# Kernel optimization log

Hardware: AMD Instinct MI355X
Metric: run time of the kernel (lower is better)

Reference implementation:

```python
import jax, jax.numpy as jnp
import numpy as np

NEG = -1e30  # log-space 'minus infinity' that stays finite in fp32 arithmetic
BLANK = 0


def _lse3(a, b, c):
    m = jnp.maximum(jnp.maximum(a, b), c)
    return m + jnp.log(jnp.exp(a - m) + jnp.exp(b - m) + jnp.exp(c - m))


def setup_inputs() -> dict:
    key = jax.random.key(0)
    k1, k2, k3, k4 = jax.random.split(key, 4)
    B, T, C, L = 16, 512, 4096, 128
    scores = jax.random.normal(k1, (B, T, C), dtype=jnp.float32)
    labels = jax.random.randint(k2, (B, L), 1, C, dtype=jnp.int64)      # no blanks in targets
    feat_lens = jax.random.randint(k3, (B,), 384, T + 1, dtype=jnp.int64)
    label_lens = jax.random.randint(k4, (B,), 64, L + 1, dtype=jnp.int64)
    return {"scores": scores, "labels": labels, "feat_lens": feat_lens, "label_lens": label_lens}


def reference(scores, labels, feat_lens, label_lens):
    # scores: [B, T, C]. Matches torch: log_softmax then nn.CTCLoss(blank=0,
    # reduction='mean', zero_infinity=True).
    scores = scores.astype(jnp.float32)
    log_probs = jax.nn.log_softmax(scores, axis=-1)                      # [B, T, C]
    B, T, C = scores.shape
    L = labels.shape[1]
    S = 2 * L + 1  # extended label: blank, l1, blank, ..., lL, blank

    ext = jnp.full((B, S), BLANK, dtype=labels.dtype).at[:, 1::2].set(labels)
    # Gather per-(t, extended-symbol) log-probs once: [B, T, S]
    lp = jnp.take_along_axis(log_probs, jnp.broadcast_to(ext[:, None, :], (B, T, S)), axis=2)

    # skip transition s-2 -> s allowed iff ext[s] != blank and ext[s] != ext[s-2]
    skip = jnp.concatenate(
        [jnp.zeros((B, 2), bool), (ext[:, 2:] != ext[:, :-2]) & (ext[:, 2:] != BLANK)], axis=1)

    alpha0 = jnp.full((B, S), NEG, dtype=jnp.float32).at[:, 0].set(lp[:, 0, 0])
    alpha0 = alpha0.at[:, 1].set(jnp.where(label_lens > 0, lp[:, 0, 1], NEG))

    lp_t_first = jnp.swapaxes(lp, 0, 1)  # [T, B, S]

    def step(alpha, xs):
        lp_t, t = xs
        a1 = jnp.pad(alpha, ((0, 0), (1, 0)), constant_values=NEG)[:, :S]
        a2 = jnp.pad(alpha, ((0, 0), (2, 0)), constant_values=NEG)[:, :S]
        a2 = jnp.where(skip, a2, NEG)
        new = lp_t + _lse3(alpha, a1, a2)
        alpha = jnp.where((t < feat_lens)[:, None], new, alpha)  # freeze past feat_len
        return alpha, None

    alpha, _ = jax.lax.scan(step, alpha0, (lp_t_first[1:], jnp.arange(1, T)))

    end = 2 * label_lens  # index of final blank per sample
    a_end = jnp.take_along_axis(alpha, end[:, None], axis=1)[:, 0]
    a_end1 = jnp.where(
        label_lens > 0,
        jnp.take_along_axis(alpha, jnp.maximum(end - 1, 0)[:, None], axis=1)[:, 0], NEG)
    m = jnp.maximum(a_end, a_end1)
    log_lik = m + jnp.log(jnp.exp(a_end - m) + jnp.exp(a_end1 - m))
    loss = -log_lik
    loss = jnp.where(loss > 0.5e30, 0.0, loss)  # zero_infinity=True
    denom = jnp.maximum(label_lens, 1).astype(loss.dtype)
    return jnp.mean(loss / denom)  # torch 'mean': divide by target_lengths, then batch mean
```

## Files before the change

kernel.cpp:

```cpp
#include <hip/hip_runtime.h>

#define T_ 512
#define C_ 4096
#define L_ 128
#define RCPLN2 1.4426950408889634f
#define LN2 0.6931471805599453f
#define NEGL (-1e30f)
#define SCALE_CTR 4.722366482869645e21f
#define SCALE_LOG 72.0f

__device__ __forceinline__ float fexp2(float x) { return __builtin_amdgcn_exp2f(x); }
__device__ __forceinline__ float flog2(float x) { return __builtin_amdgcn_logf(x); }
__device__ __forceinline__ float frcp(float x)  { return __builtin_amdgcn_rcpf(x); }
__device__ __forceinline__ float lg(float x)    { return (x > 0.f) ? flog2(x) : NEGL; }

template <int CTRL>
__device__ __forceinline__ float dppmov(float v) {
  return __int_as_float(__builtin_amdgcn_update_dpp(
      0, __float_as_int(v), CTRL, 0xF, 0xF, true));
}
__device__ __forceinline__ float wshr1(float v) { return dppmov<0x138>(v); }
__device__ __forceinline__ float wshl1(float v) { return dppmov<0x130>(v); }
template <int CTRL>
__device__ __forceinline__ float maxdpp(float v) {
  return fmaxf(v, dppmov<CTRL>(v));
}
__device__ __forceinline__ float wavemax(float v) {
  v = maxdpp<0xB1>(v);
  v = maxdpp<0x4E>(v);
  v = maxdpp<0x141>(v);
  v = maxdpp<0x140>(v);
  v = maxdpp<0x142>(v);
  v = maxdpp<0x143>(v);
  return __int_as_float(__builtin_amdgcn_readlane(__float_as_int(v), 63));
}

__global__ __launch_bounds__(256) void k_lse_gather(
    const float* __restrict__ scores, const int* __restrict__ labels,
    const int* __restrict__ feat_lens,
    float* __restrict__ p_lab, float* __restrict__ p_blank,
    int* __restrict__ dpDone, float* __restrict__ lossAcc) {
  const int row = blockIdx.x;
  const int b = row >> 9;
  const int t = row & (T_ - 1);
  if (row == 0 && threadIdx.x == 0) {
    atomicExch(dpDone, 0);
    atomicExch(lossAcc, 0.0f);
  }
  if (t >= feat_lens[b]) return;

  __shared__ float sRow[C_];
  __shared__ float sSum[4];
  const float4* __restrict__ rp4 = (const float4*)(scores + (size_t)row * C_);
  float4* sRow4 = (float4*)sRow;
  const int tid = threadIdx.x;

  float s0 = 0.f, s1 = 0.f, s2 = 0.f, s3 = 0.f;
#pragma unroll
  for (int k = 0; k < 4; ++k) {
    float4 v = rp4[tid + 256 * k];
    sRow4[tid + 256 * k] = v;
    s0 += fexp2(v.x * RCPLN2);
    s1 += fexp2(v.y * RCPLN2);
    s2 += fexp2(v.z * RCPLN2);
    s3 += fexp2(v.w * RCPLN2);
  }
  float s = (s0 + s1) + (s2 + s3);
#pragma unroll
  for (int off = 32; off; off >>= 1) s += __shfl_down(s, off);
  const int wid = tid >> 6, lane = tid & 63;
  if (lane == 0) sSum[wid] = s;
  __syncthreads();
  const float l2sum = flog2((sSum[0] + sSum[1]) + (sSum[2] + sSum[3]));

  if (tid < L_) {
    const int lab = labels[b * L_ + tid];
    p_lab[(size_t)row * L_ + tid] = fexp2(sRow[lab] * RCPLN2 - l2sum);
  } else if (tid == L_) {
    p_blank[row] = fexp2(sRow[0] * RCPLN2 - l2sum);
  }
}

#define FSTEP(cck, cbk)                                                 \
  {                                                                     \
    const float n3 = (cck).y * (a3 + a2 + (skip3 ? a1 : 0.f));          \
    const float n4 = (cbk) * (a4 + a3);      \
    const float pn = wshr1(n3);              \
    const float n0 = (cbk) * (a0 + pp);                                 \
    const float n1 = (cck).x * (a1 + a0 + (skip1 ? pp : 0.f));          \
    const float n2 = (cbk) * (a2 + a1);                                 \
    a0 = n0; a1 = n1; a2 = n2; a3 = n3;                                 \
    a4 = (lane == 63) ? n4 : 0.f;                                       \
    pp = pn;                                                            \
  }
#define FRESCALE                                                        \
  {                                                                     \
    float m = wavemax(fmaxf(fmaxf(fmaxf(a0, a1), fmaxf(a2, a3)), a4));  \
    m = fmaxf(m, 1e-35f);                     \
    const float r2 = frcp(m) * SCALE_CTR;              \
    Sa += flog2(m) - SCALE_LOG;                                         \
    a0 *= r2; a1 *= r2; a2 *= r2; a3 *= r2; a4 *= r2; pp *= r2;         \
  }
#define FPREF(PC, PB, tbase)                                            \
  {                                                                     \
    const int t0_ = min((tbase) + 0, flen - 1);                         \
    const int t1_ = min((tbase) + 1, flen - 1);                         \
    const int t2_ = min((tbase) + 2, flen - 1);                         \
    const int t3_ = min((tbase) + 3, flen - 1);                         \
    PC[0] = llp[t0_ * 64 + lane]; PB[0] = lbp[t0_];                     \
    PC[1] = llp[t1_ * 64 + lane]; PB[1] = lbp[t1_];                     \
    PC[2] = llp[t2_ * 64 + lane]; PB[2] = lbp[t2_];                     \
    PC[3] = llp[t3_ * 64 + lane]; PB[3] = lbp[t3_];                     \
  }
#define FPHASE(CC, CB, PC, PB, tb)                                      \
  if ((tb) <= tm) {                                                     \
    FPREF(PC, PB, (tb) + 12);                                           \
    FSTEP(CC[0], CB[0]); FSTEP(CC[1], CB[1]); FRESCALE;                 \
    FSTEP(CC[2], CB[2]); FSTEP(CC[3], CB[3]); FRESCALE;                 \
  }

#define BSTEP(cck, cbk)                                                 \
  {                                                                     \
    const float n0 = (cbk) * (b0 + b1);                                 \
    const float n1 = (cck).x * (b1 + b2 + (skip3 ? b3 : 0.f));          \
    const float n4 = (cbk) * b4;             \
    const float q0n = wshl1(n0);                  \
    const float q1n = wshl1(n1);                                        \
    const float n3 = (cck).y * (b3 + q0 + (skipd ? q1 : 0.f));          \
    const float n2 = (cbk) * (b2 + b3);                                 \
    b0 = n0; b1 = n1; b2 = n2; b3 = n3; b4 = n4;                        \
    q0 = (lane == 63) ? n4 : q0n;                                       \
    q1 = q1n;                                                           \
  }
#define BRESCALE                                                        \
  {                                                                     \
    float m = wavemax(fmaxf(fmaxf(fmaxf(b0, b1), fmaxf(b2, b3)), b4));  \
    m = fmaxf(m, 1e-35f);                                               \
    const float r2 = frcp(m) * SCALE_CTR;                               \
    Sb += flog2(m) - SCALE_LOG;                                         \
    b0 *= r2; b1 *= r2; b2 *= r2; b3 *= r2; b4 *= r2; q0 *= r2;         \
    q1 *= r2;                                                           \
  }
#define BPREF(PC, PB, tbase)                                            \
  {                                                                     \
    const int t0_ = max((tbase) - 0, tm);                               \
    const int t1_ = max((tbase) - 1, tm);                               \
    const int t2_ = max((tbase) - 2, tm);                               \
    const int t3_ = max((tbase) - 3, tm);                               \
    PC[0] = llp[t0_ * 64 + lane]; PB[0] = lbp[t0_];                     \
    PC[1] = llp[t1_ * 64 + lane]; PB[1] = lbp[t1_];                     \
    PC[2] = llp[t2_ * 64 + lane]; PB[2] = lbp[t2_];                     \
    PC[3] = llp[t3_ * 64 + lane]; PB[3] = lbp[t3_];                     \
  }
#define BPHASE(CC, CB, PC, PB, tb)                                      \
  if ((tb) >= tm) {                                                     \
    BPREF(PC, PB, (tb) - 12);                                           \
    if ((tb) - 0 >= tm) BSTEP(CC[0], CB[0]);                            \
    if ((tb) - 1 >= tm) BSTEP(CC[1], CB[1]);                            \
    BRESCALE;                                                           \
    if ((tb) - 2 >= tm) BSTEP(CC[2], CB[2]);                            \
    if ((tb) - 3 >= tm) BSTEP(CC[3], CB[3]);                            \
    BRESCALE;                                                           \
  }

__global__ __launch_bounds__(128) void k_ctc_dp(
    const float* __restrict__ p_lab, const float* __restrict__ p_blank,
    const int* __restrict__ labels, const int* __restrict__ feat_lens,
    const int* __restrict__ label_lens, int* __restrict__ dpDone,
    float* __restrict__ lossAcc, float* __restrict__ out, int B) {
  const int b = blockIdx.x;
  const int lane = threadIdx.x & 63;
  const int wid = threadIdx.x >> 6;
  const int flen = feat_lens[b];
  const int llen = label_lens[b];
  const int tm = (flen >> 1) & ~3;

  const int l0 = labels[b * L_ + 2 * lane];
  const int l1 = labels[b * L_ + 2 * lane + 1];
  const int lm1 = __shfl_up(l1, 1);
  const int ln0 = __shfl_down(l0, 1);
  const bool skip1 = (lane > 0) && (l0 != lm1);
  const bool skip3 = (l1 != l0);
  const bool skipd = (lane < 63) && (ln0 != l1);

  const float2* __restrict__ llp = (const float2*)(p_lab + (size_t)b * T_ * L_);
  const float* __restrict__ lpl = p_lab + (size_t)b * T_ * L_;
  const float* __restrict__ lbp = p_blank + b * T_;

  __shared__ float sB[257];
  __shared__ float sSb;

  if (wid == 0) {
    const float2 ll0 = llp[lane];
    float a0 = (lane == 0) ? lbp[0] : 0.f;
    float a1 = (lane == 0) ? ll0.x : 0.f;
    float a2 = 0.f, a3 = 0.f, a4 = 0.f;
    float pp = 0.f;
    float Sa = 0.f;

    float2 Ac[4], Bc[4], Cc[4], Dc[4];
    float Ab[4], Bb[4], Cb[4], Db[4];
    FPREF(Ac, Ab, 1);
    FPREF(Bc, Bb, 5);
    FPREF(Cc, Cb, 9);
    int t = 1;
    while (t <= tm) {
      FPHASE(Ac, Ab, Dc, Db, t);
      FPHASE(Bc, Bb, Ac, Ab, t + 4);
      FPHASE(Cc, Cb, Bc, Bb, t + 8);
      FPHASE(Dc, Db, Cc, Cb, t + 12);
      t += 16;
    }
    const float2 cce = llp[tm * 64 + lane];
    const float cbe = lbp[tm];
    const float lb2 = flog2(cbe), lc0 = flog2(cce.x), lc1 = flog2(cce.y);
    const float la0 = lg(a0), la1 = lg(a1), la2 = lg(a2), la3 = lg(a3);
    const float la4 = lg(a4);
    __syncthreads();
    float w0 = la0 + sB[4 * lane + 0] - lb2;
    float w1 = la1 + sB[4 * lane + 1] - lc0;
    float w2 = la2 + sB[4 * lane + 2] - lb2;
    float w3 = la3 + sB[4 * lane + 3] - lc1;
    float m = fmaxf(fmaxf(w0, w1), fmaxf(w2, w3));
    float w4 = NEGL;
    if (lane == 63) { w4 = la4 + sB[256] - lb2; m = fmaxf(m, w4); }
#pragma unroll
    for (int off = 1; off < 64; off <<= 1) m = fmaxf(m, __shfl_xor(m, off));
    float sum = fexp2(w0 - m) + fexp2(w1 - m) + fexp2(w2 - m) + fexp2(w3 - m);
    if (lane == 63) sum += fexp2(w4 - m);
#pragma unroll
    for (int off = 1; off < 64; off <<= 1) sum += __shfl_xor(sum, off);
    if (lane == 0) {
      const float l2lik = m + flog2(sum) + Sa + sSb;
      float loss = -LN2 * l2lik;
      if (!(fabsf(loss) < 0.5e30f)) loss = 0.0f;
      atomicAdd(lossAcc, loss / (float)llen);
      const int done = __hip_atomic_fetch_add(dpDone, 1, __ATOMIC_ACQ_REL,
                                              __HIP_MEMORY_SCOPE_AGENT);
      if (done == B - 1)
        out[0] = atomicAdd(lossAcc, 0.0f) / (float)B;
    }
  } else {
    const int e = 2 * llen;
    const float ve = lbp[flen - 1];
    const float vo = lpl[(size_t)(flen - 1) * L_ + (llen - 1)];
    float b0 = (4 * lane == e) ? ve : 0.f;
    float b1 = (4 * lane + 1 == e - 1) ? vo : 0.f;
    float b2 = (4 * lane + 2 == e) ? ve : 0.f;
    float b3 = (4 * lane + 3 == e - 1) ? vo : 0.f;
    float b4 = (lane == 63 && e == 256) ? ve : 0.f;
    float q0 = __shfl_down(b0, 1); q0 = (lane == 63) ? b4 : q0;
    float q1 = __shfl_down(b1, 1); q1 = (lane == 63) ? 0.f : q1;
    float Sb = 0.f;

    float2 Ac[4], Bc[4], Cc[4], Dc[4];
    float Ab[4], Bb[4], Cb[4], Db[4];
    int t = flen - 2;
    BPREF(Ac, Ab, t);
    BPREF(Bc, Bb, t - 4);
    BPREF(Cc, Cb, t - 8);
    while (t >= tm) {
      BPHASE(Ac, Ab, Dc, Db, t);
      BPHASE(Bc, Bb, Ac, Ab, t - 4);
      BPHASE(Cc, Cb, Bc, Bb, t - 8);
      BPHASE(Dc, Db, Cc, Cb, t - 12);
      t -= 16;
    }
    sB[4 * lane + 0] = lg(b0);
    sB[4 * lane + 1] = lg(b1);
    sB[4 * lane + 2] = lg(b2);
    sB[4 * lane + 3] = lg(b3);
    if (lane == 63) sB[256] = lg(b4);
    if (lane == 0) sSb = Sb;
    __syncthreads();
  }
}

extern "C" void kernel_launch(void* const* d_in, const int* in_sizes, int n_in,
                              void* d_out, int out_size, void* d_ws, size_t ws_size,
                              hipStream_t stream) {
  const float* scores = (const float*)d_in[0];
  const int* labels = (const int*)d_in[1];
  const int* feat_lens = (const int*)d_in[2];
  const int* label_lens = (const int*)d_in[3];
  const int B = in_sizes[2];

  int* dpDone = (int*)d_ws;
  float* lossAcc = (float*)d_ws + 1;
  float* p_lab = (float*)d_ws + 64;
  float* p_blank = p_lab + (size_t)B * T_ * L_;
  float* out = (float*)d_out;

  k_lse_gather<<<B * T_, 256, 0, stream>>>(scores, labels, feat_lens,
                                           p_lab, p_blank, dpDone, lossAcc);
  k_ctc_dp<<<B, 128, 0, stream>>>(p_lab, p_blank, labels, feat_lens, label_lens,
                                  dpDone, lossAcc, out, B);
}
```

Measured before the change: 217.8 us.

## Stage DP emission probabilities through LDS with dedicated producer waves

The CTC alpha/beta recursion waves no longer prefetch per-step probabilities from global memory into registers. Two extra producer waves now copy 24-timestep chunks into double-buffered shared memory, and the compute waves read from LDS. This is meant to take global-load latency off the serial recurrence chain. In exchange it adds a block-wide barrier per chunk that couples the forward and backward waves, plus LDS read latency on every step.

```diff
diff --git a/kernel.cpp b/kernel.cpp
--- a/kernel.cpp
+++ b/kernel.cpp
@@ -3,6 +3,7 @@
 #define T_ 512
 #define C_ 4096
 #define L_ 128
+#define R_ 24
 #define RCPLN2 1.4426950408889634f
 #define LN2 0.6931471805599453f
 #define NEGL (-1e30f)
@@ -84,8 +85,8 @@
 #define FSTEP(cck, cbk)                                                 \
   {                                                                     \
     const float n3 = (cck).y * (a3 + a2 + (skip3 ? a1 : 0.f));          \
-    const float n4 = (cbk) * (a4 + a3);      \
-    const float pn = wshr1(n3);              \
+    const float n4 = (cbk) * (a4 + a3);                                 \
+    const float pn = wshr1(n3);                                         \
     const float n0 = (cbk) * (a0 + pp);                                 \
     const float n1 = (cck).x * (a1 + a0 + (skip1 ? pp : 0.f));          \
     const float n2 = (cbk) * (a2 + a1);                                 \
@@ -96,35 +97,17 @@
 #define FRESCALE                                                        \
   {                                                                     \
     float m = wavemax(fmaxf(fmaxf(fmaxf(a0, a1), fmaxf(a2, a3)), a4));  \
-    m = fmaxf(m, 1e-35f);                     \
-    const float r2 = frcp(m) * SCALE_CTR;              \
+    m = fmaxf(m, 1e-35f);                                               \
+    const float r2 = frcp(m) * SCALE_CTR;                               \
     Sa += flog2(m) - SCALE_LOG;                                         \
     a0 *= r2; a1 *= r2; a2 *= r2; a3 *= r2; a4 *= r2; pp *= r2;         \
   }
-#define FPREF(PC, PB, tbase)                                            \
-  {                                                                     \
-    const int t0_ = min((tbase) + 0, flen - 1);                         \
-    const int t1_ = min((tbase) + 1, flen - 1);                         \
-    const int t2_ = min((tbase) + 2, flen - 1);                         \
-    const int t3_ = min((tbase) + 3, flen - 1);                         \
-    PC[0] = llp[t0_ * 64 + lane]; PB[0] = lbp[t0_];                     \
-    PC[1] = llp[t1_ * 64 + lane]; PB[1] = lbp[t1_];                     \
-    PC[2] = llp[t2_ * 64 + lane]; PB[2] = lbp[t2_];                     \
-    PC[3] = llp[t3_ * 64 + lane]; PB[3] = lbp[t3_];                     \
-  }
-#define FPHASE(CC, CB, PC, PB, tb)                                      \
-  if ((tb) <= tm) {                                                     \
-    FPREF(PC, PB, (tb) + 12);                                           \
-    FSTEP(CC[0], CB[0]); FSTEP(CC[1], CB[1]); FRESCALE;                 \
-    FSTEP(CC[2], CB[2]); FSTEP(CC[3], CB[3]); FRESCALE;                 \
-  }
-
 #define BSTEP(cck, cbk)                                                 \
   {                                                                     \
     const float n0 = (cbk) * (b0 + b1);                                 \
     const float n1 = (cck).x * (b1 + b2 + (skip3 ? b3 : 0.f));          \
-    const float n4 = (cbk) * b4;             \
-    const float q0n = wshl1(n0);                  \
+    const float n4 = (cbk) * b4;                                        \
+    const float q0n = wshl1(n0);                                        \
     const float q1n = wshl1(n1);                                        \
     const float n3 = (cck).y * (b3 + q0 + (skipd ? q1 : 0.f));          \
     const float n2 = (cbk) * (b2 + b3);                                 \
@@ -141,36 +124,80 @@
     b0 *= r2; b1 *= r2; b2 *= r2; b3 *= r2; b4 *= r2; q0 *= r2;         \
     q1 *= r2;                                                           \
   }
-#define BPREF(PC, PB, tbase)                                            \
-  {                                                                     \
-    const int t0_ = max((tbase) - 0, tm);                               \
-    const int t1_ = max((tbase) - 1, tm);                               \
-    const int t2_ = max((tbase) - 2, tm);                               \
-    const int t3_ = max((tbase) - 3, tm);                               \
-    PC[0] = llp[t0_ * 64 + lane]; PB[0] = lbp[t0_];                     \
-    PC[1] = llp[t1_ * 64 + lane]; PB[1] = lbp[t1_];                     \
-    PC[2] = llp[t2_ * 64 + lane]; PB[2] = lbp[t2_];                     \
-    PC[3] = llp[t3_ * 64 + lane]; PB[3] = lbp[t3_];                     \
-  }
-#define BPHASE(CC, CB, PC, PB, tb)                                      \
-  if ((tb) >= tm) {                                                     \
-    BPREF(PC, PB, (tb) - 12);                                           \
-    if ((tb) - 0 >= tm) BSTEP(CC[0], CB[0]);                            \
-    if ((tb) - 1 >= tm) BSTEP(CC[1], CB[1]);                            \
+
+#define FGROUP(g)                                                       \
+  if (t0f + 4 * (g) <= tm) {                                            \
+    const float2 lc0 = *(const float2*)&sF[cb][4 * (g) + 0][2 * lane];  \
+    const float2 lc1 = *(const float2*)&sF[cb][4 * (g) + 1][2 * lane];  \
+    const float2 lc2 = *(const float2*)&sF[cb][4 * (g) + 2][2 * lane];  \
+    const float2 lc3 = *(const float2*)&sF[cb][4 * (g) + 3][2 * lane];  \
+    const float lb0 = sFb[cb][4 * (g) + 0];                             \
+    const float lb1 = sFb[cb][4 * (g) + 1];                             \
+    const float lb2_ = sFb[cb][4 * (g) + 2];                            \
+    const float lb3 = sFb[cb][4 * (g) + 3];                             \
+    FSTEP(lc0, lb0); FSTEP(lc1, lb1); FRESCALE;                         \
+    FSTEP(lc2, lb2_); FSTEP(lc3, lb3); FRESCALE;                        \
+  }
+#define BGROUP(g)                                                       \
+  if (t0b - 4 * (g) >= tm) {                                            \
+    const float2 lc0 = *(const float2*)&sG[cb][4 * (g) + 0][2 * lane];  \
+    const float2 lc1 = *(const float2*)&sG[cb][4 * (g) + 1][2 * lane];  \
+    const float2 lc2 = *(const float2*)&sG[cb][4 * (g) + 2][2 * lane];  \
+    const float2 lc3 = *(const float2*)&sG[cb][4 * (g) + 3][2 * lane];  \
+    const float lb0 = sGb[cb][4 * (g) + 0];                             \
+    const float lb1 = sGb[cb][4 * (g) + 1];                             \
+    const float lb2_ = sGb[cb][4 * (g) + 2];                            \
+    const float lb3 = sGb[cb][4 * (g) + 3];                             \
+    if (t0b - 4 * (g) - 0 >= tm) BSTEP(lc0, lb0);                       \
+    if (t0b - 4 * (g) - 1 >= tm) BSTEP(lc1, lb1);                       \
     BRESCALE;                                                           \
-    if ((tb) - 2 >= tm) BSTEP(CC[2], CB[2]);                            \
-    if ((tb) - 3 >= tm) BSTEP(CC[3], CB[3]);                            \
+    if (t0b - 4 * (g) - 2 >= tm) BSTEP(lc2, lb2_);                      \
+    if (t0b - 4 * (g) - 3 >= tm) BSTEP(lc3, lb3);                       \
     BRESCALE;                                                           \
   }
 
-__global__ __launch_bounds__(128) void k_ctc_dp(
+#define STAGEF(nb, ss1)                                                 \
+  {                                                                     \
+    const int t0 = 1 + R_ * (ss1);                                      \
+    float4 v[12];                                                       \
+    _Pragma("unroll")                                                   \
+    for (int i = 0; i < 12; ++i) {                                      \
+      const int tt = min(t0 + 2 * i + h, flen - 1);                     \
+      v[i] = *(const float4*)(lpl + (size_t)tt * L_ + 4 * c);           \
+    }                                                                   \
+    const float bl = lbp[min(t0 + (int)lane, flen - 1)];                \
+    _Pragma("unroll")                                                   \
+    for (int i = 0; i < 12; ++i)                                        \
+      *(float4*)&sF[nb][2 * i + h][4 * c] = v[i];                       \
+    if (lane < R_) sFb[nb][lane] = bl;                                  \
+  }
+#define STAGEB(nb, ss1)                                                 \
+  {                                                                     \
+    const int t0 = flen - 2 - R_ * (ss1);                               \
+    float4 v[12];                                                       \
+    _Pragma("unroll")                                                   \
+    for (int i = 0; i < 12; ++i) {                                      \
+      const int tt = max(t0 - (2 * i + h), 0);                          \
+      v[i] = *(const float4*)(lpl + (size_t)tt * L_ + 4 * c);           \
+    }                                                                   \
+    const float bl = lbp[max(t0 - (int)lane, 0)];                       \
+    _Pragma("unroll")                                                   \
+    for (int i = 0; i < 12; ++i)                                        \
+      *(float4*)&sG[nb][2 * i + h][4 * c] = v[i];                       \
+    if (lane < R_) sGb[nb][lane] = bl;                                  \
+  }
+
+__global__ __launch_bounds__(256) void k_ctc_dp(
     const float* __restrict__ p_lab, const float* __restrict__ p_blank,
     const int* __restrict__ labels, const int* __restrict__ feat_lens,
     const int* __restrict__ label_lens, int* __restrict__ dpDone,
     float* __restrict__ lossAcc, float* __restrict__ out, int B) {
   const int b = blockIdx.x;
-  const int lane = threadIdx.x & 63;
-  const int wid = threadIdx.x >> 6;
+  const int tid = threadIdx.x;
+  const int lane = tid & 63;
+  const int wid = tid >> 6;
+  const int h = lane >> 5;
+  const int c = lane & 31;
   const int flen = feat_lens[b];
   const int llen = label_lens[b];
   const int tm = (flen >> 1) & ~3;
@@ -187,36 +214,72 @@
   const float* __restrict__ lpl = p_lab + (size_t)b * T_ * L_;
   const float* __restrict__ lbp = p_blank + b * T_;
 
+  __shared__ float sF[2][R_][L_];
+  __shared__ float sG[2][R_][L_];
+  __shared__ float sFb[2][R_];
+  __shared__ float sGb[2][R_];
   __shared__ float sB[257];
   __shared__ float sSb;
 
+  const int NSf = (tm + R_ - 1) / R_;
+  const int NSb = (flen - 1 - tm + R_ - 1) / R_;
+  const int NS = NSf > NSb ? NSf : NSb;
+
+  float a0 = 0.f, a1 = 0.f, a2 = 0.f, a3 = 0.f, a4 = 0.f, pp = 0.f, Sa = 0.f;
+  float b0 = 0.f, b1 = 0.f, b2 = 0.f, b3 = 0.f, b4 = 0.f, q0 = 0.f, q1 = 0.f,
+        Sb = 0.f;
   if (wid == 0) {
     const float2 ll0 = llp[lane];
-    float a0 = (lane == 0) ? lbp[0] : 0.f;
-    float a1 = (lane == 0) ? ll0.x : 0.f;
-    float a2 = 0.f, a3 = 0.f, a4 = 0.f;
-    float pp = 0.f;
-    float Sa = 0.f;
-
-    float2 Ac[4], Bc[4], Cc[4], Dc[4];
-    float Ab[4], Bb[4], Cb[4], Db[4];
-    FPREF(Ac, Ab, 1);
-    FPREF(Bc, Bb, 5);
-    FPREF(Cc, Cb, 9);
-    int t = 1;
-    while (t <= tm) {
-      FPHASE(Ac, Ab, Dc, Db, t);
-      FPHASE(Bc, Bb, Ac, Ab, t + 4);
-      FPHASE(Cc, Cb, Bc, Bb, t + 8);
-      FPHASE(Dc, Db, Cc, Cb, t + 12);
-      t += 16;
+    a0 = (lane == 0) ? lbp[0] : 0.f;
+    a1 = (lane == 0) ? ll0.x : 0.f;
+  } else if (wid == 1) {
+    const int e = 2 * llen;
+    const float ve = lbp[flen - 1];
+    const float vo = lpl[(size_t)(flen - 1) * L_ + (llen - 1)];
+    b0 = (4 * lane == e) ? ve : 0.f;
+    b1 = (4 * lane + 1 == e - 1) ? vo : 0.f;
+    b2 = (4 * lane + 2 == e) ? ve : 0.f;
+    b3 = (4 * lane + 3 == e - 1) ? vo : 0.f;
+    b4 = (lane == 63 && e == 256) ? ve : 0.f;
+    q0 = __shfl_down(b0, 1); q0 = (lane == 63) ? b4 : q0;
+    q1 = __shfl_down(b1, 1); q1 = (lane == 63) ? 0.f : q1;
+  }
+
+  if (wid == 2) STAGEF(0, 0);
+  if (wid == 3) STAGEB(0, 0);
+  __syncthreads();
+
+  for (int ss = 0; ss < NS; ++ss) {
+    const int cb = ss & 1;
+    if (wid == 0) {
+      const int t0f = 1 + R_ * ss;
+      FGROUP(0); FGROUP(1); FGROUP(2); FGROUP(3); FGROUP(4); FGROUP(5);
+    } else if (wid == 1) {
+      const int t0b = flen - 2 - R_ * ss;
+      BGROUP(0); BGROUP(1); BGROUP(2); BGROUP(3); BGROUP(4); BGROUP(5);
+    } else if (wid == 2) {
+      if (ss + 1 < NS) STAGEF((ss + 1) & 1, ss + 1);
+    } else {
+      if (ss + 1 < NS) STAGEB((ss + 1) & 1, ss + 1);
     }
+    __syncthreads();
+  }
+
+  if (wid == 1) {
+    sB[4 * lane + 0] = lg(b0);
+    sB[4 * lane + 1] = lg(b1);
+    sB[4 * lane + 2] = lg(b2);
+    sB[4 * lane + 3] = lg(b3);
+    if (lane == 63) sB[256] = lg(b4);
+    if (lane == 0) sSb = Sb;
+  }
+  __syncthreads();
+  if (wid == 0) {
     const float2 cce = llp[tm * 64 + lane];
     const float cbe = lbp[tm];
     const float lb2 = flog2(cbe), lc0 = flog2(cce.x), lc1 = flog2(cce.y);
     const float la0 = lg(a0), la1 = lg(a1), la2 = lg(a2), la3 = lg(a3);
     const float la4 = lg(a4);
-    __syncthreads();
     float w0 = la0 + sB[4 * lane + 0] - lb2;
     float w1 = la1 + sB[4 * lane + 1] - lc0;
     float w2 = la2 + sB[4 * lane + 2] - lb2;
@@ -240,39 +303,6 @@
       if (done == B - 1)
         out[0] = atomicAdd(lossAcc, 0.0f) / (float)B;
     }
-  } else {
-    const int e = 2 * llen;
-    const float ve = lbp[flen - 1];
-    const float vo = lpl[(size_t)(flen - 1) * L_ + (llen - 1)];
-    float b0 = (4 * lane == e) ? ve : 0.f;
-    float b1 = (4 * lane + 1 == e - 1) ? vo : 0.f;
-    float b2 = (4 * lane + 2 == e) ? ve : 0.f;
-    float b3 = (4 * lane + 3 == e - 1) ? vo : 0.f;
-    float b4 = (lane == 63 && e == 256) ? ve : 0.f;
-    float q0 = __shfl_down(b0, 1); q0 = (lane == 63) ? b4 : q0;
-    float q1 = __shfl_down(b1, 1); q1 = (lane == 63) ? 0.f : q1;
-    float Sb = 0.f;
-
-    float2 Ac[4], Bc[4], Cc[4], Dc[4];
-    float Ab[4], Bb[4], Cb[4], Db[4];
-    int t = flen - 2;
-    BPREF(Ac, Ab, t);
-    BPREF(Bc, Bb, t - 4);
-    BPREF(Cc, Cb, t - 8);
-    while (t >= tm) {
-      BPHASE(Ac, Ab, Dc, Db, t);
-      BPHASE(Bc, Bb, Ac, Ab, t - 4);
-      BPHASE(Cc, Cb, Bc, Bb, t - 8);
-      BPHASE(Dc, Db, Cc, Cb, t - 12);
-      t -= 16;
-    }
-    sB[4 * lane + 0] = lg(b0);
-    sB[4 * lane + 1] = lg(b1);
-    sB[4 * lane + 2] = lg(b2);
-    sB[4 * lane + 3] = lg(b3);
-    if (lane == 63) sB[256] = lg(b4);
-    if (lane == 0) sSb = Sb;
-    __syncthreads();
   }
 }
 
@@ -293,6 +323,6 @@
 
   k_lse_gather<<<B * T_, 256, 0, stream>>>(scores, labels, feat_lens,
                                            p_lab, p_blank, dpDone, lossAcc);
-  k_ctc_dp<<<B, 128, 0, stream>>>(p_lab, p_blank, labels, feat_lens, label_lens,
+  k_ctc_dp<<<B, 256, 0, stream>>>(p_lab, p_blank, labels, feat_lens, label_lens,
                                   dpDone, lossAcc, out, B);
 }
```

Measured after the change: 217.0 us. About the same (-0.4%).
